# Performance work log

Measured on AMD Instinct MI355X. Metric: run time of the kernel, lower is better.

## Reference

```python
import jax, jax.numpy as jnp
import numpy as np
from jax import lax

N_LAYERS = 10
N_BLOCKS = 3
N_STACK = N_LAYERS * N_BLOCKS  # 30
WIDTH = 512
SKIP_W = 256
CH = 1
QUANT = 256
BOTTLENECK = 16
KSIZE = 3
SCALE = 2 ** (N_LAYERS - 1)  # 512, nearest upsample factor
B, T = 1, 16384
T_EMB = T // SCALE  # 32


def causal_conv(x, w, b, dilation):
    # x: [B,Cin,T], w: [Cout,Cin,K] -> causal dilated conv, output [B,Cout,T]
    k = w.shape[-1]
    pad = (k - 1) * dilation
    y = lax.conv_general_dilated(x, w, window_strides=(1,), padding=[(pad, 0)],
                                 rhs_dilation=(dilation,),
                                 dimension_numbers=('NCH', 'OIH', 'NCH'))
    return y + b[None, :, None]


def conv1x1(x, w, b):
    # x: [B,Cin,T], w: [Cout,Cin]
    return jnp.einsum('oc,bct->bot', w, x) + b[None, :, None]


def setup_inputs() -> dict:
    key = jax.random.key(0)
    ks = jax.random.split(key, 24)
    s = 0.05
    inp = {
        'x': jax.random.normal(ks[0], (B, CH, T), jnp.float32),
        'embedding': jax.random.normal(ks[1], (B, BOTTLENECK, T_EMB), jnp.float32),
        'w_init': jax.random.normal(ks[2], (WIDTH, CH, KSIZE), jnp.float32) * s,
        'b_init': jnp.zeros((WIDTH,), jnp.float32),
        'w_iskip': jax.random.normal(ks[3], (SKIP_W, WIDTH), jnp.float32) * s,
        'b_iskip': jnp.zeros((SKIP_W,), jnp.float32),
        'w_dil': jax.random.normal(ks[4], (N_STACK, 2 * WIDTH, WIDTH, KSIZE), jnp.float32) * s,
        'b_dil': jnp.zeros((N_STACK, 2 * WIDTH), jnp.float32),
        'w_cond': jax.random.normal(ks[5], (N_STACK, 2 * WIDTH, BOTTLENECK), jnp.float32) * s,
        'b_cond': jnp.zeros((N_STACK, 2 * WIDTH), jnp.float32),
        'w_res': jax.random.normal(ks[6], (N_STACK, WIDTH, WIDTH), jnp.float32) * s,
        'b_res': jnp.zeros((N_STACK, WIDTH), jnp.float32),
        'w_skip': jax.random.normal(ks[7], (N_STACK, SKIP_W, WIDTH), jnp.float32) * s,
        'b_skip': jnp.zeros((N_STACK, SKIP_W), jnp.float32),
        'w_fskip': jax.random.normal(ks[8], (SKIP_W, SKIP_W), jnp.float32) * s,
        'b_fskip': jnp.zeros((SKIP_W,), jnp.float32),
        'w_fcond': jax.random.normal(ks[9], (SKIP_W, BOTTLENECK), jnp.float32) * s,
        'b_fcond': jnp.zeros((SKIP_W,), jnp.float32),
        'w_quant': jax.random.normal(ks[10], (QUANT, SKIP_W), jnp.float32) * s,
        'b_quant': jnp.zeros((QUANT,), jnp.float32),
    }
    return inp


def reference(x, embedding, w_init, b_init, w_iskip, b_iskip, w_dil, b_dil,
              w_cond, b_cond, w_res, b_res, w_skip, b_skip,
              w_fskip, b_fskip, w_fcond, b_fcond, w_quant, b_quant):
    # initial causal conv (kernel 3, dilation 1) + initial skip 1x1
    h = causal_conv(x, w_init, b_init, 1)            # [B,WIDTH,T]
    skip = conv1x1(h, w_iskip, b_iskip)              # [B,SKIP_W,T]
    for i in range(N_STACK):
        dilation = 2 ** (i % N_LAYERS)
        cond = conv1x1(embedding, w_cond[i], b_cond[i])      # [B,2W,T_EMB]
        cond_up = jnp.repeat(cond, SCALE, axis=-1)           # nearest upsample -> [B,2W,T]
        dilated = causal_conv(h, w_dil[i], b_dil[i], dilation) + cond_up
        filters = jax.nn.sigmoid(dilated[:, :WIDTH, :])
        gates = jnp.tanh(dilated[:, WIDTH:, :])
        pre = filters * gates
        h = h + conv1x1(pre, w_res[i], b_res[i])
        skip = skip + conv1x1(pre, w_skip[i], b_skip[i])
    skip = conv1x1(jax.nn.relu(skip), w_fskip, b_fskip)
    fcond = jnp.repeat(conv1x1(embedding, w_fcond, b_fcond), SCALE, axis=-1)
    skip = skip + fcond
    return conv1x1(jax.nn.relu(skip), w_quant, b_quant)     # [B,QUANT,T]
```

## Files before the change

### kernel.cpp

```cpp
#include <hip/hip_runtime.h>


typedef _Float16 f16x8 __attribute__((ext_vector_type(8)));
typedef float f32x4 __attribute__((ext_vector_type(4)));

#define NSTACK 30
#define TLEN   16384

typedef __attribute__((address_space(1))) const unsigned int glob_u32;
typedef __attribute__((address_space(3))) unsigned int lds_u32;

__device__ __forceinline__ void gll16(const unsigned short* g, unsigned short* l) {
  __builtin_amdgcn_global_load_lds((glob_u32*)g, (lds_u32*)l, 16, 0, 0);
}

__device__ __forceinline__ unsigned short f2h(float x) {
  union { _Float16 h; unsigned short u; } c;
  c.h = (_Float16)x;
  return c.u;
}
__device__ __forceinline__ unsigned pack2(float a, float b) {
  return (unsigned)f2h(a) | ((unsigned)f2h(b) << 16);
}
__device__ __forceinline__ f16x8 ldh(const unsigned short* p) {
  return *(const f16x8*)p;
}
__device__ __forceinline__ float sigmoidf_(float x){ return 1.0f/(1.0f+__expf(-x)); }
__device__ __forceinline__ float tanhf_(float x){ return 1.0f - 2.0f/(__expf(2.0f*x)+1.0f); }
#define MFMA16(a,b,c) __builtin_amdgcn_mfma_f32_16x16x32_f16((a),(b),(c),0,0,0)


__global__ void cast_f16_kernel(const float* __restrict__ src,
                                unsigned short* __restrict__ dst, int n4) {
  int g = blockIdx.x*256 + threadIdx.x;
  if (g >= n4) return;
  f32x4 v = *(const f32x4*)(src + 4*(size_t)g);
  unsigned int* d = (unsigned int*)(dst + 4*(size_t)g);
  d[0] = pack2(v[0], v[1]);
  d[1] = pack2(v[2], v[3]);
}

__global__ void transpose_wdil_kernel(const float* __restrict__ src,
                                      unsigned short* __restrict__ dst) {
  int g = blockIdx.x*256 + threadIdx.x;
  if (g >= NSTACK*1024*512) return;
  int c = g & 511;
  int m = (g >> 9) & 1023;
  int i = g >> 19;
  const float* s = src + (size_t)g*3;
  #pragma unroll
  for (int tap=0; tap<3; ++tap)
    dst[(((size_t)i*3+tap)*1024 + m)*512 + c] = f2h(s[tap]);
}

__global__ void cond_kernel(const float* __restrict__ emb,
                            const float* __restrict__ w_cond, const float* __restrict__ b_cond,
                            const float* __restrict__ b_dil,
                            const float* __restrict__ w_fcond, const float* __restrict__ b_fcond,
                            float* __restrict__ cond_all, float* __restrict__ fcond_all) {
  int g = blockIdx.x*256 + threadIdx.x;
  if (g < NSTACK*1024) {
    float acc[32];
    float base = b_cond[g] + b_dil[g];
    #pragma unroll
    for (int e=0;e<32;++e) acc[e] = base;
    #pragma unroll
    for (int c=0;c<16;++c) {
      float wv = w_cond[(size_t)g*16 + c];
      #pragma unroll
      for (int e=0;e<32;++e) acc[e] += wv * emb[c*32+e];
    }
    #pragma unroll
    for (int e=0;e<32;++e) cond_all[(size_t)g*32+e] = acc[e];
  } else if (g < NSTACK*1024 + 256) {
    int m = g - NSTACK*1024;
    float acc[32];
    float base = b_fcond[m];
    #pragma unroll
    for (int e=0;e<32;++e) acc[e] = base;
    #pragma unroll
    for (int c=0;c<16;++c) {
      float wv = w_fcond[(size_t)m*16 + c];
      #pragma unroll
      for (int e=0;e<32;++e) acc[e] += wv * emb[c*32+e];
    }
    #pragma unroll
    for (int e=0;e<32;++e) fcond_all[(size_t)m*32+e] = acc[e];
  }
}

__global__ void h0_kernel(const float* __restrict__ x, const float* __restrict__ w_init,
                          const float* __restrict__ b_init,
                          float* __restrict__ h_f32, unsigned short* __restrict__ h_h16) {
  int g = blockIdx.x*256 + threadIdx.x;
  int t = g >> 7;
  int c = (g & 127) << 2;
  float xm2 = (t>=2)? x[t-2] : 0.f;
  float xm1 = (t>=1)? x[t-1] : 0.f;
  float x0  = x[t];
  f32x4 hv;
  #pragma unroll
  for (int r=0;r<4;++r) {
    int cc = c + r;
    hv[r] = w_init[cc*3+0]*xm2 + w_init[cc*3+1]*xm1 + w_init[cc*3+2]*x0 + b_init[cc];
  }
  *(f32x4*)&h_f32[(size_t)t*512 + c] = hv;
  unsigned int* hb = (unsigned int*)&h_h16[(size_t)t*512 + c];
  hb[0] = pack2(hv[0],hv[1]); hb[1] = pack2(hv[2],hv[3]);
}

__global__ __launch_bounds__(512) void skip_init_kernel(
    const unsigned short* __restrict__ h_h16, const unsigned short* __restrict__ Wiskip,
    const float* __restrict__ b_iskip, float* __restrict__ skip_f32) {
  int tid=threadIdx.x, w=tid>>6, l=tid&63, lr=l&15, lc=l>>4;
  int tb = blockIdx.x<<6;
  f32x4 acc[2][4];
  #pragma unroll
  for (int mf=0;mf<2;++mf)
    #pragma unroll
    for (int nf=0;nf<4;++nf) acc[mf][nf] = {0.f,0.f,0.f,0.f};
  for (int kc=0;kc<512;kc+=32) {
    f16x8 b[4];
    #pragma unroll
    for (int nf=0;nf<4;++nf)
      b[nf] = ldh(&h_h16[(size_t)(tb+16*nf+lr)*512 + kc + lc*8]);
    #pragma unroll
    for (int mf=0;mf<2;++mf) {
      f16x8 a = ldh(&Wiskip[(size_t)(w*32+16*mf+lr)*512 + kc + lc*8]);
      #pragma unroll
      for (int nf=0;nf<4;++nf)
        acc[mf][nf] = MFMA16(a, b[nf], acc[mf][nf]);
    }
  }
  #pragma unroll
  for (int mf=0;mf<2;++mf)
    #pragma unroll
    for (int nf=0;nf<4;++nf) {
      int s0 = w*32+16*mf+4*lc;
      int t  = tb+16*nf+lr;
      f32x4 v;
      #pragma unroll
      for (int r=0;r<4;++r) v[r] = acc[mf][nf][r] + b_iskip[s0+r];
      *(f32x4*)&skip_f32[(size_t)t*256+s0] = v;
    }
}

__global__ __launch_bounds__(256, 4) void dil_kernel(
    const unsigned short* __restrict__ h_in,
    unsigned short* __restrict__ pre,
    const unsigned short* __restrict__ A_dil,
    const float* __restrict__ cond,
    const unsigned short* __restrict__ zerobuf,
    int dilation) {
  __shared__ unsigned short Ab[2][128][32];
  __shared__ unsigned short Bb[2][128][32];
  const int tid = threadIdx.x;
  const int w = tid >> 6, l = tid & 63;
  const int lr = l & 15, lc = l >> 4;
  const int nt = blockIdx.x & 127, mt = blockIdx.x >> 7;
  const int tb = nt << 7;
  const int e  = tb >> 9;
  const int wr = w >> 1, wc = w & 1;

  const int srowA0 = (w<<5) + (l>>2);
  const int schunk = (l & 3) << 3;

  f32x4 fa[2][4], ga[2][4];
  #pragma unroll
  for (int mf=0;mf<2;++mf)
    #pragma unroll
    for (int nf=0;nf<4;++nf) { fa[mf][nf] = {0.f,0.f,0.f,0.f}; ga[mf][nf] = {0.f,0.f,0.f,0.f}; }

  auto stage = [&](int buf, int s){
    const int tap = s >> 4;
    const int kc  = (s & 15) << 5;
    const int shift = (2 - tap) * dilation;
    const unsigned short* Abase = A_dil + (size_t)tap * (1024*512) + kc + schunk;
    #pragma unroll
    for (int j=0;j<2;++j){
      const int r = srowA0 + (j<<4);
      const int m = mt*64 + r + ((r>>6)*448);
      gll16(Abase + (size_t)m*512, &Ab[buf][(w<<5)+(j<<4)][0]);
      const int t = tb + r - shift;
      const unsigned short* srcB = (t >= 0) ? (h_in + (size_t)t*512 + kc + schunk)
                                            : (zerobuf + schunk);
      gll16(srcB, &Bb[buf][(w<<5)+(j<<4)][0]);
    }
  };

  stage(0, 0);
  for (int s=0; s<48; ++s) {
    const int cur = s & 1;
    __syncthreads();
    if (s+1 < 48) stage(cur^1, s+1);
    f16x8 af[2], ag[2], bf[4];
    #pragma unroll
    for (int mf=0;mf<2;++mf){
      const int row = (wr<<5) + (mf<<4) + lr;
      af[mf] = ldh(&Ab[cur][row][lc<<3]);
      ag[mf] = ldh(&Ab[cur][64+row][lc<<3]);
    }
    #pragma unroll
    for (int nf=0;nf<4;++nf)
      bf[nf] = ldh(&Bb[cur][(wc<<6)+(nf<<4)+lr][lc<<3]);
    #pragma unroll
    for (int mf=0;mf<2;++mf)
      #pragma unroll
      for (int nf=0;nf<4;++nf){
        fa[mf][nf] = MFMA16(af[mf], bf[nf], fa[mf][nf]);
        ga[mf][nf] = MFMA16(ag[mf], bf[nf], ga[mf][nf]);
      }
  }

  #pragma unroll
  for (int mf=0;mf<2;++mf)
    #pragma unroll
    for (int nf=0;nf<4;++nf){
      const int m0 = mt*64 + (wr<<5) + (mf<<4) + (lc<<2);
      const int t  = tb + (wc<<6) + (nf<<4) + lr;
      float pv[4];
      #pragma unroll
      for (int r=0;r<4;++r){
        float f = fa[mf][nf][r] + cond[(size_t)(m0+r)*32 + e];
        float g = ga[mf][nf][r] + cond[(size_t)(m0+r+512)*32 + e];
        pv[r] = sigmoidf_(f) * tanhf_(g);
      }
      unsigned int* pp = (unsigned int*)&pre[(size_t)t*512 + m0];
      pp[0] = pack2(pv[0], pv[1]);
      pp[1] = pack2(pv[2], pv[3]);
    }
}

__global__ __launch_bounds__(256, 3) void ressk_kernel(
    const unsigned short* __restrict__ pre,
    unsigned short* __restrict__ h_out,
    float* __restrict__ h_f32,
    float* __restrict__ skip_f32,
    const unsigned short* __restrict__ Wres,
    const unsigned short* __restrict__ Wskip,
    const float* __restrict__ b_res,
    const float* __restrict__ b_skip) {
  __shared__ unsigned short Ab[2][128][32];
  __shared__ unsigned short Bb[2][128][32];
  const int tid = threadIdx.x;
  const int w = tid >> 6, l = tid & 63;
  const int lr = l & 15, lc = l >> 4;
  const int nt = blockIdx.x & 127, mt = blockIdx.x >> 7;
  const int tb = nt << 7;
  const int wr = w >> 1, wc = w & 1;
  const bool isres = (mt < 4);
  const unsigned short* W = isres ? Wres : Wskip;
  const int mrow0 = (isres ? mt : (mt-4)) * 128;

  const int srowA0 = (w<<5) + (l>>2);
  const int schunk = (l & 3) << 3;

  f32x4 acc[4][4];
  #pragma unroll
  for (int mf=0;mf<4;++mf)
    #pragma unroll
    for (int nf=0;nf<4;++nf) acc[mf][nf] = {0.f,0.f,0.f,0.f};

  auto stage = [&](int buf, int s){
    const int kc = s << 5;
    #pragma unroll
    for (int j=0;j<2;++j){
      const int r = srowA0 + (j<<4);
      gll16(W + (size_t)(mrow0 + r)*512 + kc + schunk, &Ab[buf][(w<<5)+(j<<4)][0]);
      gll16(pre + (size_t)(tb + r)*512 + kc + schunk, &Bb[buf][(w<<5)+(j<<4)][0]);
    }
  };

  stage(0, 0);
  for (int s=0; s<16; ++s) {
    const int cur = s & 1;
    __syncthreads();
    if (s+1 < 16) stage(cur^1, s+1);
    f16x8 a[4], bf[4];
    #pragma unroll
    for (int mf=0;mf<4;++mf)
      a[mf] = ldh(&Ab[cur][(wr<<6)+(mf<<4)+lr][lc<<3]);
    #pragma unroll
    for (int nf=0;nf<4;++nf)
      bf[nf] = ldh(&Bb[cur][(wc<<6)+(nf<<4)+lr][lc<<3]);
    #pragma unroll
    for (int mf=0;mf<4;++mf)
      #pragma unroll
      for (int nf=0;nf<4;++nf)
        acc[mf][nf] = MFMA16(a[mf], bf[nf], acc[mf][nf]);
  }

  if (isres) {
    #pragma unroll
    for (int mf=0;mf<4;++mf)
      #pragma unroll
      for (int nf=0;nf<4;++nf){
        const int m0 = mrow0 + (wr<<6) + (mf<<4) + (lc<<2);
        const int t  = tb + (wc<<6) + (nf<<4) + lr;
        f32x4* hp = (f32x4*)&h_f32[(size_t)t*512 + m0];
        f32x4 hv = *hp;
        #pragma unroll
        for (int r=0;r<4;++r) hv[r] += acc[mf][nf][r] + b_res[m0+r];
        *hp = hv;
        unsigned int* hb = (unsigned int*)&h_out[(size_t)t*512 + m0];
        hb[0] = pack2(hv[0],hv[1]); hb[1] = pack2(hv[2],hv[3]);
      }
  } else {
    #pragma unroll
    for (int mf=0;mf<4;++mf)
      #pragma unroll
      for (int nf=0;nf<4;++nf){
        const int s0 = mrow0 + (wr<<6) + (mf<<4) + (lc<<2);
        const int t  = tb + (wc<<6) + (nf<<4) + lr;
        f32x4* sp = (f32x4*)&skip_f32[(size_t)t*256 + s0];
        f32x4 sv = *sp;
        #pragma unroll
        for (int r=0;r<4;++r) sv[r] += acc[mf][nf][r] + b_skip[s0+r];
        *sp = sv;
      }
  }
}

__global__ __launch_bounds__(512) void final_kernel(
    const float* __restrict__ skip_f32, const unsigned short* __restrict__ Wfs,
    const float* __restrict__ b_fskip, const float* __restrict__ fcond,
    const unsigned short* __restrict__ Wq, const float* __restrict__ b_quant,
    float* __restrict__ out) {
  __shared__ unsigned short S1[64][264];
  __shared__ unsigned short S2[64][264];
  int tid=threadIdx.x, w=tid>>6, l=tid&63, lr=l&15, lc=l>>4;
  int tb = blockIdx.x<<6, e = tb>>9;

  for (int j = tid; j < 64*64; j += 512) {
    int r  = j >> 6;
    int c4 = (j & 63) << 2;
    f32x4 v = *(const f32x4*)&skip_f32[(size_t)(tb+r)*256 + c4];
    #pragma unroll
    for (int q=0;q<4;++q) v[q] = fmaxf(v[q], 0.f);
    unsigned int* sp = (unsigned int*)&S1[r][c4];
    sp[0] = pack2(v[0],v[1]); sp[1] = pack2(v[2],v[3]);
  }
  __syncthreads();

  f32x4 acc[2][4];
  #pragma unroll
  for (int mf=0;mf<2;++mf)
    #pragma unroll
    for (int nf=0;nf<4;++nf) acc[mf][nf] = {0.f,0.f,0.f,0.f};
  for (int kc=0;kc<256;kc+=32) {
    f16x8 b[4];
    #pragma unroll
    for (int nf=0;nf<4;++nf) b[nf] = ldh(&S1[16*nf+lr][kc + lc*8]);
    #pragma unroll
    for (int mf=0;mf<2;++mf) {
      f16x8 a = ldh(&Wfs[(size_t)(w*32+16*mf+lr)*256 + kc + lc*8]);
      #pragma unroll
      for (int nf=0;nf<4;++nf)
        acc[mf][nf] = MFMA16(a, b[nf], acc[mf][nf]);
    }
  }
  #pragma unroll
  for (int mf=0;mf<2;++mf)
    #pragma unroll
    for (int nf=0;nf<4;++nf) {
      int m0 = w*32+16*mf+4*lc;
      int n  = 16*nf+lr;
      float pv[4];
      #pragma unroll
      for (int r=0;r<4;++r) {
        float v = acc[mf][nf][r] + b_fskip[m0+r] + fcond[(size_t)(m0+r)*32 + e];
        pv[r] = fmaxf(v, 0.f);
      }
      unsigned int* pp = (unsigned int*)&S2[n][m0];
      pp[0] = pack2(pv[0],pv[1]); pp[1] = pack2(pv[2],pv[3]);
    }
  __syncthreads();

  f32x4 acc2[2][4];
  #pragma unroll
  for (int mf=0;mf<2;++mf)
    #pragma unroll
    for (int nf=0;nf<4;++nf) acc2[mf][nf] = {0.f,0.f,0.f,0.f};
  for (int kc=0;kc<256;kc+=32) {
    f16x8 b[4];
    #pragma unroll
    for (int nf=0;nf<4;++nf) b[nf] = ldh(&S2[16*nf+lr][kc + lc*8]);
    #pragma unroll
    for (int mf=0;mf<2;++mf) {
      f16x8 a = ldh(&Wq[(size_t)(w*32+16*mf+lr)*256 + kc + lc*8]);
      #pragma unroll
      for (int nf=0;nf<4;++nf)
        acc2[mf][nf] = MFMA16(a, b[nf], acc2[mf][nf]);
    }
  }
  #pragma unroll
  for (int mf=0;mf<2;++mf)
    #pragma unroll
    for (int nf=0;nf<4;++nf) {
      int q0 = w*32+16*mf+4*lc;
      int t  = tb + 16*nf + lr;
      #pragma unroll
      for (int r=0;r<4;++r)
        out[(size_t)(q0+r)*TLEN + t] = acc2[mf][nf][r] + b_quant[q0+r];
    }
}


extern "C" void kernel_launch(void* const* d_in, const int* in_sizes, int n_in,
                              void* d_out, int out_size, void* d_ws, size_t ws_size,
                              hipStream_t stream) {
  const float* x       = (const float*)d_in[0];
  const float* emb     = (const float*)d_in[1];
  const float* w_init  = (const float*)d_in[2];
  const float* b_init  = (const float*)d_in[3];
  const float* w_iskip = (const float*)d_in[4];
  const float* b_iskip = (const float*)d_in[5];
  const float* w_dil   = (const float*)d_in[6];
  const float* b_dil   = (const float*)d_in[7];
  const float* w_cond  = (const float*)d_in[8];
  const float* b_cond  = (const float*)d_in[9];
  const float* w_res   = (const float*)d_in[10];
  const float* b_res   = (const float*)d_in[11];
  const float* w_skip  = (const float*)d_in[12];
  const float* b_skip  = (const float*)d_in[13];
  const float* w_fskip = (const float*)d_in[14];
  const float* b_fskip = (const float*)d_in[15];
  const float* w_fcond = (const float*)d_in[16];
  const float* b_fcond = (const float*)d_in[17];
  const float* w_quant = (const float*)d_in[18];
  const float* b_quant = (const float*)d_in[19];
  float* out = (float*)d_out;

  char* ws = (char*)d_ws;
  size_t off = 0;
  auto carve = [&](size_t bytes) -> void* {
    void* p = ws + off;
    off += (bytes + 255) & ~(size_t)255;
    return p;
  };
  unsigned short* A_dil     = (unsigned short*)carve((size_t)NSTACK*3*1024*512*2);
  unsigned short* Wres_h    = (unsigned short*)carve((size_t)NSTACK*512*512*2);
  unsigned short* Wskip_h   = (unsigned short*)carve((size_t)NSTACK*256*512*2);
  unsigned short* Wiskip_h  = (unsigned short*)carve((size_t)256*512*2);
  unsigned short* Wfskip_h  = (unsigned short*)carve((size_t)256*256*2);
  unsigned short* Wquant_h  = (unsigned short*)carve((size_t)256*256*2);
  float*          h_f32     = (float*)carve((size_t)TLEN*512*4);
  unsigned short* h_h16     = (unsigned short*)carve((size_t)2*TLEN*512*2);
  unsigned short* pre_h16   = (unsigned short*)carve((size_t)TLEN*512*2);
  float*          skip_f32  = (float*)carve((size_t)TLEN*256*4);
  float*          cond_all  = (float*)carve((size_t)NSTACK*1024*32*4);
  float*          fcond_all = (float*)carve((size_t)256*32*4);
  unsigned short* zerobuf   = (unsigned short*)carve((size_t)512*2);
  if (off > ws_size) return;

  hipMemsetAsync(zerobuf, 0, 512*2, stream);

  cast_f16_kernel<<<(NSTACK*512*512/4 + 255)/256, 256, 0, stream>>>(w_res,   Wres_h,   NSTACK*512*512/4);
  cast_f16_kernel<<<(NSTACK*256*512/4 + 255)/256, 256, 0, stream>>>(w_skip,  Wskip_h,  NSTACK*256*512/4);
  cast_f16_kernel<<<(256*512/4 + 255)/256,        256, 0, stream>>>(w_iskip, Wiskip_h, 256*512/4);
  cast_f16_kernel<<<(256*256/4 + 255)/256,        256, 0, stream>>>(w_fskip, Wfskip_h, 256*256/4);
  cast_f16_kernel<<<(256*256/4 + 255)/256,        256, 0, stream>>>(w_quant, Wquant_h, 256*256/4);
  transpose_wdil_kernel<<<(NSTACK*1024*512 + 255)/256, 256, 0, stream>>>(w_dil, A_dil);
  cond_kernel<<<(NSTACK*1024 + 256 + 255)/256, 256, 0, stream>>>(
      emb, w_cond, b_cond, b_dil, w_fcond, b_fcond, cond_all, fcond_all);

  h0_kernel<<<TLEN*128/256, 256, 0, stream>>>(x, w_init, b_init, h_f32, h_h16);
  skip_init_kernel<<<TLEN/64, 512, 0, stream>>>(h_h16, Wiskip_h, b_iskip, skip_f32);

  const size_t HB = (size_t)TLEN*512;
  for (int i = 0; i < NSTACK; ++i) {
    int d = 1 << (i % 10);
    dil_kernel<<<1024, 256, 0, stream>>>(
        h_h16 + (size_t)(i & 1)*HB,
        pre_h16,
        A_dil + (size_t)i*3*1024*512,
        cond_all + (size_t)i*1024*32,
        zerobuf,
        d);
    ressk_kernel<<<768, 256, 0, stream>>>(
        pre_h16,
        h_h16 + (size_t)((i + 1) & 1)*HB,
        h_f32, skip_f32,
        Wres_h + (size_t)i*512*512,
        Wskip_h + (size_t)i*256*512,
        b_res + (size_t)i*512,
        b_skip + (size_t)i*256);
  }

  final_kernel<<<TLEN/64, 512, 0, stream>>>(
      skip_f32, Wfskip_h, b_fskip, fcond_all, Wquant_h, b_quant, out);
}
```

Before: 3.313 ms.

## Fuse dilated conv and res/skip GEMMs into one kernel with per-tile flags

Merges the per-layer dilated-conv/gating kernel and the residual/skip 1x1 kernel into a single launch. Every block first computes its slice of the gated activations and bumps a per-time-tile counter. The first six M-tiles of each time tile then spin on that counter until all eight producer blocks are done, and run the res/skip GEMM. This removes one launch per layer and lets the second GEMM start as soon as its time tile is ready, without waiting for a grid-wide kernel boundary. In exchange it relies on all 1024 blocks being resident at once to avoid deadlock, and spinning blocks hold compute slots.

```diff
diff --git a/kernel.cpp b/kernel.cpp
--- a/kernel.cpp
+++ b/kernel.cpp
@@ -28,6 +28,14 @@
 __device__ __forceinline__ float sigmoidf_(float x){ return 1.0f/(1.0f+__expf(-x)); }
 __device__ __forceinline__ float tanhf_(float x){ return 1.0f - 2.0f/(__expf(2.0f*x)+1.0f); }
 #define MFMA16(a,b,c) __builtin_amdgcn_mfma_f32_16x16x32_f16((a),(b),(c),0,0,0)
+
+__device__ __forceinline__ void spin_ge(int* p, int v){
+  while (__hip_atomic_load(p, __ATOMIC_ACQUIRE, __HIP_MEMORY_SCOPE_AGENT) < v)
+    __builtin_amdgcn_s_sleep(2);
+}
+__device__ __forceinline__ void flag_add(int* p){
+  __hip_atomic_fetch_add(p, 1, __ATOMIC_RELEASE, __HIP_MEMORY_SCOPE_AGENT);
+}
 
 
 __global__ void cast_f16_kernel(const float* __restrict__ src,
@@ -145,13 +153,21 @@
     }
 }
 
-__global__ __launch_bounds__(256, 4) void dil_kernel(
+__global__ __launch_bounds__(256, 4) void layer_fused_kernel(
     const unsigned short* __restrict__ h_in,
+    unsigned short* __restrict__ h_out,
+    float* __restrict__ h_f32,
     unsigned short* __restrict__ pre,
+    float* __restrict__ skip_f32,
     const unsigned short* __restrict__ A_dil,
+    const unsigned short* __restrict__ Wres,
+    const unsigned short* __restrict__ Wskip,
     const float* __restrict__ cond,
+    const float* __restrict__ b_res,
+    const float* __restrict__ b_skip,
     const unsigned short* __restrict__ zerobuf,
-    int dilation) {
+    int dilation,
+    int* __restrict__ pre_cnt) {
   __shared__ unsigned short Ab[2][128][32];
   __shared__ unsigned short Bb[2][128][32];
   const int tid = threadIdx.x;
@@ -165,95 +181,83 @@
   const int srowA0 = (w<<5) + (l>>2);
   const int schunk = (l & 3) << 3;
 
-  f32x4 fa[2][4], ga[2][4];
-  #pragma unroll
-  for (int mf=0;mf<2;++mf)
-    #pragma unroll
-    for (int nf=0;nf<4;++nf) { fa[mf][nf] = {0.f,0.f,0.f,0.f}; ga[mf][nf] = {0.f,0.f,0.f,0.f}; }
-
-  auto stage = [&](int buf, int s){
-    const int tap = s >> 4;
-    const int kc  = (s & 15) << 5;
-    const int shift = (2 - tap) * dilation;
-    const unsigned short* Abase = A_dil + (size_t)tap * (1024*512) + kc + schunk;
-    #pragma unroll
-    for (int j=0;j<2;++j){
-      const int r = srowA0 + (j<<4);
-      const int m = mt*64 + r + ((r>>6)*448);
-      gll16(Abase + (size_t)m*512, &Ab[buf][(w<<5)+(j<<4)][0]);
-      const int t = tb + r - shift;
-      const unsigned short* srcB = (t >= 0) ? (h_in + (size_t)t*512 + kc + schunk)
-                                            : (zerobuf + schunk);
-      gll16(srcB, &Bb[buf][(w<<5)+(j<<4)][0]);
-    }
-  };
-
-  stage(0, 0);
-  for (int s=0; s<48; ++s) {
-    const int cur = s & 1;
-    __syncthreads();
-    if (s+1 < 48) stage(cur^1, s+1);
-    f16x8 af[2], ag[2], bf[4];
-    #pragma unroll
-    for (int mf=0;mf<2;++mf){
-      const int row = (wr<<5) + (mf<<4) + lr;
-      af[mf] = ldh(&Ab[cur][row][lc<<3]);
-      ag[mf] = ldh(&Ab[cur][64+row][lc<<3]);
-    }
-    #pragma unroll
-    for (int nf=0;nf<4;++nf)
-      bf[nf] = ldh(&Bb[cur][(wc<<6)+(nf<<4)+lr][lc<<3]);
+  {
+    f32x4 fa[2][4], ga[2][4];
     #pragma unroll
     for (int mf=0;mf<2;++mf)
       #pragma unroll
+      for (int nf=0;nf<4;++nf) { fa[mf][nf] = {0.f,0.f,0.f,0.f}; ga[mf][nf] = {0.f,0.f,0.f,0.f}; }
+
+    auto stage = [&](int buf, int s){
+      const int tap = s >> 4;
+      const int kc  = (s & 15) << 5;
+      const int shift = (2 - tap) * dilation;
+      const unsigned short* Abase = A_dil + (size_t)tap * (1024*512) + kc + schunk;
+      #pragma unroll
+      for (int j=0;j<2;++j){
+        const int r = srowA0 + (j<<4);
+        const int m = mt*64 + r + ((r>>6)*448);
+        gll16(Abase + (size_t)m*512, &Ab[buf][(w<<5)+(j<<4)][0]);
+        const int t = tb + r - shift;
+        const unsigned short* srcB = (t >= 0) ? (h_in + (size_t)t*512 + kc + schunk)
+                                              : (zerobuf + schunk);
+        gll16(srcB, &Bb[buf][(w<<5)+(j<<4)][0]);
+      }
+    };
+
+    stage(0, 0);
+    for (int s=0; s<48; ++s) {
+      const int cur = s & 1;
+      __syncthreads();
+      if (s+1 < 48) stage(cur^1, s+1);
+      f16x8 af[2], ag[2], bf[4];
+      #pragma unroll
+      for (int mf=0;mf<2;++mf){
+        const int row = (wr<<5) + (mf<<4) + lr;
+        af[mf] = ldh(&Ab[cur][row][lc<<3]);
+        ag[mf] = ldh(&Ab[cur][64+row][lc<<3]);
+      }
+      #pragma unroll
+      for (int nf=0;nf<4;++nf)
+        bf[nf] = ldh(&Bb[cur][(wc<<6)+(nf<<4)+lr][lc<<3]);
+      #pragma unroll
+      for (int mf=0;mf<2;++mf)
+        #pragma unroll
+        for (int nf=0;nf<4;++nf){
+          fa[mf][nf] = MFMA16(af[mf], bf[nf], fa[mf][nf]);
+          ga[mf][nf] = MFMA16(ag[mf], bf[nf], ga[mf][nf]);
+        }
+    }
+
+    #pragma unroll
+    for (int mf=0;mf<2;++mf)
+      #pragma unroll
       for (int nf=0;nf<4;++nf){
-        fa[mf][nf] = MFMA16(af[mf], bf[nf], fa[mf][nf]);
-        ga[mf][nf] = MFMA16(ag[mf], bf[nf], ga[mf][nf]);
-      }
-  }
-
-  #pragma unroll
-  for (int mf=0;mf<2;++mf)
-    #pragma unroll
-    for (int nf=0;nf<4;++nf){
-      const int m0 = mt*64 + (wr<<5) + (mf<<4) + (lc<<2);
-      const int t  = tb + (wc<<6) + (nf<<4) + lr;
-      float pv[4];
-      #pragma unroll
-      for (int r=0;r<4;++r){
-        float f = fa[mf][nf][r] + cond[(size_t)(m0+r)*32 + e];
-        float g = ga[mf][nf][r] + cond[(size_t)(m0+r+512)*32 + e];
-        pv[r] = sigmoidf_(f) * tanhf_(g);
-      }
-      unsigned int* pp = (unsigned int*)&pre[(size_t)t*512 + m0];
-      pp[0] = pack2(pv[0], pv[1]);
-      pp[1] = pack2(pv[2], pv[3]);
-    }
-}
-
-__global__ __launch_bounds__(256, 3) void ressk_kernel(
-    const unsigned short* __restrict__ pre,
-    unsigned short* __restrict__ h_out,
-    float* __restrict__ h_f32,
-    float* __restrict__ skip_f32,
-    const unsigned short* __restrict__ Wres,
-    const unsigned short* __restrict__ Wskip,
-    const float* __restrict__ b_res,
-    const float* __restrict__ b_skip) {
-  __shared__ unsigned short Ab[2][128][32];
-  __shared__ unsigned short Bb[2][128][32];
-  const int tid = threadIdx.x;
-  const int w = tid >> 6, l = tid & 63;
-  const int lr = l & 15, lc = l >> 4;
-  const int nt = blockIdx.x & 127, mt = blockIdx.x >> 7;
-  const int tb = nt << 7;
-  const int wr = w >> 1, wc = w & 1;
-  const bool isres = (mt < 4);
+        const int m0 = mt*64 + (wr<<5) + (mf<<4) + (lc<<2);
+        const int t  = tb + (wc<<6) + (nf<<4) + lr;
+        float pv[4];
+        #pragma unroll
+        for (int r=0;r<4;++r){
+          float f = fa[mf][nf][r] + cond[(size_t)(m0+r)*32 + e];
+          float g = ga[mf][nf][r] + cond[(size_t)(m0+r+512)*32 + e];
+          pv[r] = sigmoidf_(f) * tanhf_(g);
+        }
+        unsigned int* pp = (unsigned int*)&pre[(size_t)t*512 + m0];
+        pp[0] = pack2(pv[0], pv[1]);
+        pp[1] = pack2(pv[2], pv[3]);
+      }
+  }
+  __syncthreads();
+  if (tid == 0){ __threadfence(); flag_add(&pre_cnt[nt]); }
+
+  if (mt >= 6) return;
+  const int rk = mt;
+  const bool isres = (rk < 4);
   const unsigned short* W = isres ? Wres : Wskip;
-  const int mrow0 = (isres ? mt : (mt-4)) * 128;
-
-  const int srowA0 = (w<<5) + (l>>2);
-  const int schunk = (l & 3) << 3;
+  const int mrow0 = (isres ? rk : (rk-4)) * 128;
+
+  if (tid == 0) spin_ge(&pre_cnt[nt], 8);
+  __syncthreads();
 
   f32x4 acc[4][4];
   #pragma unroll
@@ -261,7 +265,7 @@
     #pragma unroll
     for (int nf=0;nf<4;++nf) acc[mf][nf] = {0.f,0.f,0.f,0.f};
 
-  auto stage = [&](int buf, int s){
+  auto stage2 = [&](int buf, int s){
     const int kc = s << 5;
     #pragma unroll
     for (int j=0;j<2;++j){
@@ -271,11 +275,11 @@
     }
   };
 
-  stage(0, 0);
+  stage2(0, 0);
   for (int s=0; s<16; ++s) {
     const int cur = s & 1;
     __syncthreads();
-    if (s+1 < 16) stage(cur^1, s+1);
+    if (s+1 < 16) stage2(cur^1, s+1);
     f16x8 a[4], bf[4];
     #pragma unroll
     for (int mf=0;mf<4;++mf)
@@ -451,9 +455,11 @@
   float*          cond_all  = (float*)carve((size_t)NSTACK*1024*32*4);
   float*          fcond_all = (float*)carve((size_t)256*32*4);
   unsigned short* zerobuf   = (unsigned short*)carve((size_t)512*2);
+  int*            flags     = (int*)carve((size_t)NSTACK*128*4);
   if (off > ws_size) return;
 
   hipMemsetAsync(zerobuf, 0, 512*2, stream);
+  hipMemsetAsync(flags, 0, (size_t)NSTACK*128*4, stream);
 
   cast_f16_kernel<<<(NSTACK*512*512/4 + 255)/256, 256, 0, stream>>>(w_res,   Wres_h,   NSTACK*512*512/4);
   cast_f16_kernel<<<(NSTACK*256*512/4 + 255)/256, 256, 0, stream>>>(w_skip,  Wskip_h,  NSTACK*256*512/4);
@@ -470,21 +476,21 @@
   const size_t HB = (size_t)TLEN*512;
   for (int i = 0; i < NSTACK; ++i) {
     int d = 1 << (i % 10);
-    dil_kernel<<<1024, 256, 0, stream>>>(
+    layer_fused_kernel<<<1024, 256, 0, stream>>>(
         h_h16 + (size_t)(i & 1)*HB,
+        h_h16 + (size_t)((i + 1) & 1)*HB,
+        h_f32,
         pre_h16,
+        skip_f32,
         A_dil + (size_t)i*3*1024*512,
-        cond_all + (size_t)i*1024*32,
-        zerobuf,
-        d);
-    ressk_kernel<<<768, 256, 0, stream>>>(
-        pre_h16,
-        h_h16 + (size_t)((i + 1) & 1)*HB,
-        h_f32, skip_f32,
         Wres_h + (size_t)i*512*512,
         Wskip_h + (size_t)i*256*512,
+        cond_all + (size_t)i*1024*32,
         b_res + (size_t)i*512,
-        b_skip + (size_t)i*256);
+        b_skip + (size_t)i*256,
+        zerobuf,
+        d,
+        flags + (size_t)i*128);
   }
 
   final_kernel<<<TLEN/64, 512, 0, stream>>>(
```

New measurement: 7.046 ms. +112.6%, slower.
